# Kernel tuning notes

Hardware: AMD Instinct MI355X
Metric: run time of the kernel (lower is better)

The kernel has to match this reference:

```python
import jax, jax.numpy as jnp
import numpy as np

EPS = 1e-5
K = 20

def _bn(x, g, b, m, v, caxis):
    shape = [1] * x.ndim
    shape[caxis] = x.shape[caxis]
    rs = lambda p: p.reshape(shape)
    return (x - rs(m)) * (rs(g) / jnp.sqrt(rs(v) + EPS)) + rs(b)

def _lrelu(x):
    return jnp.where(x > 0, x, 0.2 * x)

def _graph_feature(x, k):
    # x: [B, C, N] -> [B, N, k, 2C]
    xt = jnp.swapaxes(x, 1, 2)                       # [B, N, C]
    xx = jnp.sum(x * x, axis=1)                      # [B, N]
    dist = xx[:, :, None] + xx[:, None, :] - 2.0 * jnp.einsum('bnc,bmc->bnm', xt, xt)
    _, idx = jax.lax.top_k(-dist, k)                 # smallest distances, [B, N, k]
    nbr = jax.vmap(lambda t, i: t[i])(xt, idx)       # [B, N, k, C]
    center = xt[:, :, None, :]
    return jnp.concatenate([jnp.broadcast_to(center, nbr.shape), nbr - center], axis=-1)

def _edgeconv(x, W, g, b, m, v, k):
    feat = _graph_feature(x, k)                      # [B, N, k, 2C]
    y = jnp.einsum('bnkc,oc->bonk', feat, W)         # 1x1 conv2d
    y = _lrelu(_bn(y, g, b, m, v, caxis=1))
    return jnp.max(y, axis=-1)                       # [B, O, N]


def setup_inputs() -> dict:
    key = jax.random.key(0)
    ks = jax.random.split(key, 40)
    d = {}
    d['x'] = jax.random.normal(ks[0], (8, 3, 2048), dtype=jnp.float32)
    def mk_w(k_, o, i):
        return jax.random.normal(k_, (o, i), dtype=jnp.float32) * (1.0 / np.sqrt(i))
    def mk_bn(k_, c, pfx, out):
        k1, k2, k3, k4 = jax.random.split(k_, 4)
        out[pfx + '_g'] = jax.random.normal(k1, (c,), jnp.float32) * 0.1 + 1.0
        out[pfx + '_b'] = jax.random.normal(k2, (c,), jnp.float32) * 0.1
        out[pfx + '_m'] = jax.random.normal(k3, (c,), jnp.float32) * 0.1
        out[pfx + '_v'] = jax.random.uniform(k4, (c,), jnp.float32) + 0.5
    d['W1'] = mk_w(ks[1], 64, 6);    mk_bn(ks[2], 64, 'bn1', d)
    d['W2'] = mk_w(ks[3], 64, 128);  mk_bn(ks[4], 64, 'bn2', d)
    d['W3'] = mk_w(ks[5], 128, 128); mk_bn(ks[6], 128, 'bn3', d)
    d['W4'] = mk_w(ks[7], 256, 256); mk_bn(ks[8], 256, 'bn4', d)
    d['W5'] = mk_w(ks[9], 1024, 512); mk_bn(ks[10], 1024, 'bn5', d)
    d['L1'] = mk_w(ks[11], 512, 2048); mk_bn(ks[12], 512, 'bn6', d)
    d['L2'] = mk_w(ks[13], 256, 512);  mk_bn(ks[14], 256, 'bn7', d)
    d['L3'] = mk_w(ks[15], 40, 256)
    d['L3_b'] = jax.random.normal(ks[16], (40,), jnp.float32) * 0.01
    return d


def reference(x, W1, bn1_g, bn1_b, bn1_m, bn1_v,
              W2, bn2_g, bn2_b, bn2_m, bn2_v,
              W3, bn3_g, bn3_b, bn3_m, bn3_v,
              W4, bn4_g, bn4_b, bn4_m, bn4_v,
              W5, bn5_g, bn5_b, bn5_m, bn5_v,
              L1, bn6_g, bn6_b, bn6_m, bn6_v,
              L2, bn7_g, bn7_b, bn7_m, bn7_v,
              L3, L3_b):
    x1 = _edgeconv(x,  W1, bn1_g, bn1_b, bn1_m, bn1_v, K)   # [B, 64, N]
    x2 = _edgeconv(x1, W2, bn2_g, bn2_b, bn2_m, bn2_v, K)   # [B, 64, N]
    x3 = _edgeconv(x2, W3, bn3_g, bn3_b, bn3_m, bn3_v, K)   # [B, 128, N]
    x4 = _edgeconv(x3, W4, bn4_g, bn4_b, bn4_m, bn4_v, K)   # [B, 256, N]
    xc = jnp.concatenate([x1, x2, x3, x4], axis=1)          # [B, 512, N]
    emb = _lrelu(_bn(jnp.einsum('bcn,oc->bon', xc, W5), bn5_g, bn5_b, bn5_m, bn5_v, caxis=1))
    feat = jnp.concatenate([jnp.max(emb, axis=-1), jnp.mean(emb, axis=-1)], axis=1)  # [B, 2048]
    h = _lrelu(_bn(feat @ L1.T, bn6_g, bn6_b, bn6_m, bn6_v, caxis=1))
    h = _lrelu(_bn(h @ L2.T, bn7_g, bn7_b, bn7_m, bn7_v, caxis=1))
    return h @ L3.T + L3_b
```

## Files before the change

kernel.cpp:

```cpp
#include <hip/hip_runtime.h>
#include <math.h>

#define NPTS 2048
#define KNN 20
#define EPS_BN 1e-5f

__global__ __launch_bounds__(256) void xx_kernel(const float* __restrict__ xin,
                                                 long bstride,
                                                 float* __restrict__ xx, int C) {
    int b = blockIdx.y;
    int n = blockIdx.x * 256 + threadIdx.x;
    const float* xb = xin + (long)b * bstride;
    float s = 0.f;
    for (int c = 0; c < C; ++c) {
        float v = xb[(long)c * NPTS + n];
        s = fmaf(v, v, s);
    }
    xx[(long)b * NPTS + n] = s;
}

__global__ __launch_bounds__(512) void dist_topk_kernel(const float* __restrict__ xin,
                                                        long bstride,
                                                        const float* __restrict__ xx,
                                                        int* __restrict__ idxout, int C) {
    __shared__ float dist_s[8 * NPTS];
    int b = blockIdx.y;
    int n0 = blockIdx.x * 8;
    int tid = threadIdx.x;
    const float* xb = xin + (long)b * bstride;

    float acc[8][4];
#pragma unroll
    for (int r = 0; r < 8; ++r)
#pragma unroll
        for (int q = 0; q < 4; ++q) acc[r][q] = 0.f;

    for (int c = 0; c < C; ++c) {
        const float* row = xb + (long)c * NPTS;
        float4 xm4 = *(const float4*)(row + 4 * tid);
        float xm[4] = {xm4.x, xm4.y, xm4.z, xm4.w};
#pragma unroll
        for (int r = 0; r < 8; ++r) {
            float xnv = row[n0 + r];
#pragma unroll
            for (int q = 0; q < 4; ++q) acc[r][q] = fmaf(xnv, xm[q], acc[r][q]);
        }
    }

    const float* xxb = xx + (long)b * NPTS;
    float4 xxm4 = *(const float4*)(xxb + 4 * tid);
    float xxm[4] = {xxm4.x, xxm4.y, xxm4.z, xxm4.w};
    float xxn[8];
#pragma unroll
    for (int r = 0; r < 8; ++r) xxn[r] = xxb[n0 + r];

#pragma unroll
    for (int r = 0; r < 8; ++r) {
        float4 d;
        d.x = xxn[r] + xxm[0] - 2.f * acc[r][0];
        d.y = xxn[r] + xxm[1] - 2.f * acc[r][1];
        d.z = xxn[r] + xxm[2] - 2.f * acc[r][2];
        d.w = xxn[r] + xxm[3] - 2.f * acc[r][3];
        *(float4*)(dist_s + r * NPTS + 4 * tid) = d;
    }
    __syncthreads();

    int wave = tid >> 6, lane = tid & 63;
    int n = n0 + wave;
    float v[32];
#pragma unroll
    for (int i = 0; i < 32; ++i) v[i] = dist_s[wave * NPTS + lane + 64 * i];
    int* outp = idxout + ((long)b * NPTS + n) * KNN;

    float* wls = dist_s + wave * NPTS;

    float lm = v[0];
#pragma unroll
    for (int i = 1; i < 32; ++i) lm = fminf(lm, v[i]);
    wls[lane] = lm;
    int rk = 0;
#pragma unroll
    for (int j = 0; j < 64; ++j) {
        float lj = wls[j];
        rk += (lj < lm || (lj == lm && j < lane)) ? 1 : 0;
    }
    unsigned long long bm19 = __ballot(rk == 19);
    int src19 = (int)__ffsll((long long)bm19) - 1;
    float T = __shfl(lm, src19, 64);

    float* cand_v = wls + 256;
    int* cand_i = (int*)(wls + 320);
    int base = 0;
#pragma unroll
    for (int i = 0; i < 32; ++i) {
        bool pred = v[i] <= T;
        unsigned long long mask = __ballot(pred);
        int prefix = __builtin_amdgcn_mbcnt_hi(
            (unsigned)(mask >> 32),
            __builtin_amdgcn_mbcnt_lo((unsigned)mask, 0));
        if (pred) {
            int pos = base + prefix;
            if (pos < 64) { cand_v[pos] = v[i]; cand_i[pos] = lane + 64 * i; }
        }
        base += (int)__popcll(mask);
    }
    int M = base;

    if (M <= 64) {
        bool valid = lane < M;
        float cv = valid ? cand_v[lane] : 0.f;
        int ci = valid ? cand_i[lane] : 0;
        unsigned u = __float_as_uint(cv);
        unsigned su = (u & 0x80000000u) ? ~u : (u | 0x80000000u);
        unsigned long long key =
            valid ? (((unsigned long long)su << 32) | (unsigned)ci) : ~0ull;
        unsigned long long* key_s = (unsigned long long*)(wls + 384);
        key_s[lane] = key;
        int rk2 = 0;
#pragma unroll
        for (int j = 0; j < 64; ++j) rk2 += (key_s[j] < key) ? 1 : 0;
        bool win = valid && (rk2 < KNN);
        unsigned long long wm = __ballot(win);
        int prefix = __builtin_amdgcn_mbcnt_hi(
            (unsigned)(wm >> 32),
            __builtin_amdgcn_mbcnt_lo((unsigned)wm, 0));
        if (win) outp[prefix] = ci;
    } else {
        for (int kk = 0; kk < KNN; ++kk) {
            float bv = v[0];
            int bi = 0;
#pragma unroll
            for (int i = 1; i < 32; ++i)
                if (v[i] < bv) { bv = v[i]; bi = i; }
            int bm = lane + 64 * bi;
#pragma unroll
            for (int off = 32; off >= 1; off >>= 1) {
                float ov = __shfl_xor(bv, off, 64);
                int om = __shfl_xor(bm, off, 64);
                if (ov < bv || (ov == bv && om < bm)) { bv = ov; bm = om; }
            }
            if (lane == 0) outp[kk] = bm;
#pragma unroll
            for (int i = 0; i < 32; ++i)
                if (bm == lane + 64 * i) v[i] = 3.0e38f;
        }
    }
}

__global__ __launch_bounds__(256) void gemm_tu_kernel(
    const float* __restrict__ xin, long bstride, const float* __restrict__ W,
    const float* __restrict__ bg, const float* __restrict__ bb,
    const float* __restrict__ bm, const float* __restrict__ bv,
    float* __restrict__ tbuf, float* __restrict__ ubuf, int C, int O) {
    __shared__ float wa_s[128 * 16];
    __shared__ float wb_s[128 * 16];
    int b = blockIdx.z;
    int o0 = blockIdx.y * 16;
    int n0 = blockIdx.x * 256;
    int tid = threadIdx.x;

    for (int i = tid; i < C * 16; i += 256) {
        int c = i >> 4, ol = i & 15;
        float w1 = W[(long)(o0 + ol) * (2 * C) + c];
        float w2 = W[(long)(o0 + ol) * (2 * C) + C + c];
        wa_s[i] = w1 - w2;
        wb_s[i] = w2;
    }
    __syncthreads();

    float ta[16], ua[16];
#pragma unroll
    for (int ol = 0; ol < 16; ++ol) { ta[ol] = 0.f; ua[ol] = 0.f; }

    const float* xb = xin + (long)b * bstride;
    for (int c = 0; c < C; ++c) {
        float xv = xb[(long)c * NPTS + n0 + tid];
        const float* wac = wa_s + c * 16;
        const float* wbc = wb_s + c * 16;
#pragma unroll
        for (int ol = 0; ol < 16; ++ol) {
            ta[ol] = fmaf(wac[ol], xv, ta[ol]);
            ua[ol] = fmaf(wbc[ol], xv, ua[ol]);
        }
    }

#pragma unroll
    for (int ol = 0; ol < 16; ++ol) {
        int o = o0 + ol;
        float sc = bg[o] / sqrtf(bv[o] + EPS_BN);
        float bias = bb[o] - bm[o] * sc;
        long base = ((long)b * O + o) * NPTS + n0 + tid;
        tbuf[base] = ta[ol] * sc + bias;
        ubuf[base] = ua[ol] * sc;
    }
}

__global__ __launch_bounds__(256) void gather_kernel(const float* __restrict__ tbuf,
                                                     const float* __restrict__ ubuf,
                                                     const int* __restrict__ idx,
                                                     float* __restrict__ out, int O) {
    __shared__ float urow[NPTS];
    int o = blockIdx.x, half = blockIdx.y, b = blockIdx.z;
    int tid = threadIdx.x;
    const float4* up4 = (const float4*)(ubuf + ((long)b * O + o) * NPTS);
    float4* ur4 = (float4*)urow;
    for (int i = tid; i < NPTS / 4; i += 256) ur4[i] = up4[i];
    __syncthreads();

    const float* tp = tbuf + ((long)b * O + o) * NPTS;
    float* op = out + (long)b * (512 * NPTS) + (long)o * NPTS;
    int n = half * 1024 + tid * 4;
    float4 tv4 = *(const float4*)(tp + n);
    float tv[4] = {tv4.x, tv4.y, tv4.z, tv4.w};
    float res[4];
#pragma unroll
    for (int q = 0; q < 4; ++q) {
        const int4* ip = (const int4*)(idx + ((long)b * NPTS + n + q) * KNN);
        float mx = -3.0e38f;
#pragma unroll
        for (int jj = 0; jj < 5; ++jj) {
            int4 i4 = ip[jj];
            float y0 = tv[q] + urow[i4.x];
            float y1 = tv[q] + urow[i4.y];
            float y2 = tv[q] + urow[i4.z];
            float y3 = tv[q] + urow[i4.w];
            y0 = y0 > 0.f ? y0 : 0.2f * y0;
            y1 = y1 > 0.f ? y1 : 0.2f * y1;
            y2 = y2 > 0.f ? y2 : 0.2f * y2;
            y3 = y3 > 0.f ? y3 : 0.2f * y3;
            mx = fmaxf(mx, fmaxf(fmaxf(y0, y1), fmaxf(y2, y3)));
        }
        res[q] = mx;
    }
    *(float4*)(op + n) = make_float4(res[0], res[1], res[2], res[3]);
}

__global__ __launch_bounds__(512) void w5_reduce_kernel(
    const float* __restrict__ xc, const float* __restrict__ W5,
    const float* __restrict__ bg, const float* __restrict__ bb,
    const float* __restrict__ bm, const float* __restrict__ bv,
    float* __restrict__ pmax, float* __restrict__ psum) {
    __shared__ float w_s[512 * 16];
    __shared__ float rmax[8][16];
    __shared__ float rsum[8][16];
    int b = blockIdx.z;
    int half = blockIdx.y;
    int o0 = blockIdx.x * 16;
    int tid = threadIdx.x;

    for (int i = tid; i < 512 * 16; i += 512) {
        int c = i >> 4, ol = i & 15;
        w_s[i] = W5[(long)(o0 + ol) * 512 + c];
    }
    __syncthreads();

    float acc[2][16];
#pragma unroll
    for (int v = 0; v < 2; ++v)
#pragma unroll
        for (int ol = 0; ol < 16; ++ol) acc[v][ol] = 0.f;

    const float* xb = xc + (long)b * 512 * NPTS + half * 1024;
    for (int c = 0; c < 512; ++c) {
        float2 xv = *(const float2*)(xb + (long)c * NPTS + 2 * tid);
        const float* wc = w_s + c * 16;
#pragma unroll
        for (int ol = 0; ol < 16; ++ol) {
            float w = wc[ol];
            acc[0][ol] = fmaf(w, xv.x, acc[0][ol]);
            acc[1][ol] = fmaf(w, xv.y, acc[1][ol]);
        }
    }

    float mx[16], sm[16];
#pragma unroll
    for (int ol = 0; ol < 16; ++ol) {
        int o = o0 + ol;
        float sc = bg[o] / sqrtf(bv[o] + EPS_BN);
        float bi = bb[o] - bm[o] * sc;
        float y0 = acc[0][ol] * sc + bi;
        float y1 = acc[1][ol] * sc + bi;
        y0 = y0 > 0.f ? y0 : 0.2f * y0;
        y1 = y1 > 0.f ? y1 : 0.2f * y1;
        mx[ol] = fmaxf(y0, y1);
        sm[ol] = y0 + y1;
    }

    int wave = tid >> 6, lane = tid & 63;
#pragma unroll
    for (int ol = 0; ol < 16; ++ol) {
        float m = mx[ol], s = sm[ol];
#pragma unroll
        for (int off = 32; off >= 1; off >>= 1) {
            m = fmaxf(m, __shfl_xor(m, off, 64));
            s += __shfl_xor(s, off, 64);
        }
        mx[ol] = m;
        sm[ol] = s;
    }
    if (lane == 0) {
#pragma unroll
        for (int ol = 0; ol < 16; ++ol) { rmax[wave][ol] = mx[ol]; rsum[wave][ol] = sm[ol]; }
    }
    __syncthreads();
    if (tid < 16) {
        float m = rmax[0][tid], s = rsum[0][tid];
#pragma unroll
        for (int w = 1; w < 8; ++w) { m = fmaxf(m, rmax[w][tid]); s += rsum[w][tid]; }
        long base = ((long)half * 8 + b) * 1024 + o0 + tid;
        pmax[base] = m;
        psum[base] = s;
    }
}

__global__ __launch_bounds__(256) void w5_combine_kernel(const float* __restrict__ pmax,
                                                         const float* __restrict__ psum,
                                                         float* __restrict__ feat) {
    int b = blockIdx.x;
    for (int o = threadIdx.x; o < 1024; o += 256) {
        float m = fmaxf(pmax[(long)b * 1024 + o], pmax[(long)(8 + b) * 1024 + o]);
        float s = psum[(long)b * 1024 + o] + psum[(long)(8 + b) * 1024 + o];
        feat[(long)b * 2048 + o] = m;
        feat[(long)b * 2048 + 1024 + o] = s * (1.f / 2048.f);
    }
}

__global__ __launch_bounds__(256) void fc_kernel(const float* __restrict__ in,
                                                 const float* __restrict__ W,
                                                 const float* __restrict__ bg,
                                                 const float* __restrict__ bb,
                                                 const float* __restrict__ bm,
                                                 const float* __restrict__ bv,
                                                 float* __restrict__ out, int I, int O,
                                                 int do_lrelu) {
    int b = blockIdx.y;
    int o = blockIdx.x * 4 + (threadIdx.x >> 6);
    int lane = threadIdx.x & 63;
    if (o < O) {
        const float* ip = in + (long)b * I;
        const float* wp = W + (long)o * I;
        float s = 0.f;
        for (int i = lane; i < I; i += 64) s = fmaf(ip[i], wp[i], s);
#pragma unroll
        for (int off = 32; off >= 1; off >>= 1) s += __shfl_xor(s, off, 64);
        if (lane == 0) {
            float y;
            if (bg) {
                float scv = bg[o] / sqrtf(bv[o] + EPS_BN);
                y = (s - bm[o]) * scv + bb[o];
                if (do_lrelu) y = y > 0.f ? y : 0.2f * y;
            } else {
                y = s + bb[o];
            }
            out[(long)b * O + o] = y;
        }
    }
}

extern "C" void kernel_launch(void* const* d_in, const int* in_sizes, int n_in,
                              void* d_out, int out_size, void* d_ws, size_t ws_size,
                              hipStream_t stream) {
    const float* x = (const float*)d_in[0];
    const float* W1 = (const float*)d_in[1];
    const float* W2 = (const float*)d_in[6];
    const float* W3 = (const float*)d_in[11];
    const float* W4 = (const float*)d_in[16];
    const float* W5 = (const float*)d_in[21];
    const float* L1 = (const float*)d_in[26];
    const float* L2 = (const float*)d_in[31];
    const float* L3 = (const float*)d_in[36];
    const float* L3b = (const float*)d_in[37];

    float* xc = (float*)d_ws;
    float* tb = xc + (long)8 * 512 * NPTS;
    float* ub = tb + (long)8 * 256 * NPTS;
    int* idx = (int*)(ub + (long)8 * 256 * NPTS);
    float* xxb = (float*)(idx + (long)8 * NPTS * KNN);
    float* feat = xxb + (long)8 * NPTS;
    float* h1 = feat + (long)8 * NPTS;
    float* h2 = h1 + (long)8 * 512;
    float* pmax = tb;
    float* psum = tb + (long)2 * 8 * 1024;

    struct Layer {
        const float* xin; long bstride; const float* W;
        const float *g, *b, *m, *v; int C, O, c0;
    };
    Layer layers[4] = {
        {x, (long)3 * NPTS, W1,
         (const float*)d_in[2], (const float*)d_in[3], (const float*)d_in[4], (const float*)d_in[5],
         3, 64, 0},
        {xc, (long)512 * NPTS, W2,
         (const float*)d_in[7], (const float*)d_in[8], (const float*)d_in[9], (const float*)d_in[10],
         64, 64, 64},
        {xc + (long)64 * NPTS, (long)512 * NPTS, W3,
         (const float*)d_in[12], (const float*)d_in[13], (const float*)d_in[14], (const float*)d_in[15],
         64, 128, 128},
        {xc + (long)128 * NPTS, (long)512 * NPTS, W4,
         (const float*)d_in[17], (const float*)d_in[18], (const float*)d_in[19], (const float*)d_in[20],
         128, 256, 256},
    };

    for (int l = 0; l < 4; ++l) {
        const Layer& L = layers[l];
        xx_kernel<<<dim3(NPTS / 256, 8), 256, 0, stream>>>(L.xin, L.bstride, xxb, L.C);
        dist_topk_kernel<<<dim3(NPTS / 8, 8), 512, 0, stream>>>(L.xin, L.bstride, xxb, idx, L.C);
        gemm_tu_kernel<<<dim3(NPTS / 256, L.O / 16, 8), 256, 0, stream>>>(
            L.xin, L.bstride, L.W, L.g, L.b, L.m, L.v, tb, ub, L.C, L.O);
        gather_kernel<<<dim3(L.O, 2, 8), 256, 0, stream>>>(tb, ub, idx, xc + (long)L.c0 * NPTS, L.O);
    }

    w5_reduce_kernel<<<dim3(1024 / 16, 2, 8), 512, 0, stream>>>(
        xc, W5, (const float*)d_in[22], (const float*)d_in[23], (const float*)d_in[24],
        (const float*)d_in[25], pmax, psum);
    w5_combine_kernel<<<dim3(8), 256, 0, stream>>>(pmax, psum, feat);

    fc_kernel<<<dim3(512 / 4, 8), 256, 0, stream>>>(
        feat, L1, (const float*)d_in[27], (const float*)d_in[28], (const float*)d_in[29],
        (const float*)d_in[30], h1, 2048, 512, 1);
    fc_kernel<<<dim3(256 / 4, 8), 256, 0, stream>>>(
        h1, L2, (const float*)d_in[32], (const float*)d_in[33], (const float*)d_in[34],
        (const float*)d_in[35], h2, 512, 256, 1);
    fc_kernel<<<dim3(10, 8), 256, 0, stream>>>(
        h2, L3, nullptr, L3b, nullptr, nullptr, (float*)d_out, 256, 40, 0);
}
```

Before: 1.026 ms.

## Run W5 embedding GEMM on bf16 MFMA with split hi/lo precision

Replaces the scalar FP32 W5 reduction kernel with an MFMA-based GEMM that uses a three-product bf16 hi/lo split to approximate FP32 accuracy. It adds kernels that convert W5 and transpose and convert the concatenated features into bf16 hi/lo layouts, plus precomputation of the BN scale and bias. The goal is to move the largest dense matmul onto matrix cores. The cost is extra conversion and transpose passes, more memory traffic for the split operands, and a wider 32-way partial max/sum combine.

```diff
diff --git a/kernel.cpp b/kernel.cpp
--- a/kernel.cpp
+++ b/kernel.cpp
@@ -4,6 +4,18 @@
 #define NPTS 2048
 #define KNN 20
 #define EPS_BN 1e-5f
+
+typedef unsigned short ushort;
+typedef __attribute__((ext_vector_type(8))) short short8;
+typedef __attribute__((ext_vector_type(4))) float float4v;
+
+__device__ inline ushort bf16_rne(float x) {
+    unsigned u = __float_as_uint(x);
+    return (ushort)((u + 0x7fffu + ((u >> 16) & 1u)) >> 16);
+}
+__device__ inline float bf16_to_f(ushort h) {
+    return __uint_as_float(((unsigned)h) << 16);
+}
 
 __global__ __launch_bounds__(256) void xx_kernel(const float* __restrict__ xin,
                                                  long bstride,
@@ -235,81 +247,145 @@
     *(float4*)(op + n) = make_float4(res[0], res[1], res[2], res[3]);
 }
 
-__global__ __launch_bounds__(512) void w5_reduce_kernel(
-    const float* __restrict__ xc, const float* __restrict__ W5,
-    const float* __restrict__ bg, const float* __restrict__ bb,
-    const float* __restrict__ bm, const float* __restrict__ bv,
-    float* __restrict__ pmax, float* __restrict__ psum) {
-    __shared__ float w_s[512 * 16];
-    __shared__ float rmax[8][16];
-    __shared__ float rsum[8][16];
-    int b = blockIdx.z;
-    int half = blockIdx.y;
-    int o0 = blockIdx.x * 16;
+__global__ __launch_bounds__(256) void transpose_convert_kernel(
+    const float* __restrict__ xc, ushort* __restrict__ xh, ushort* __restrict__ xl) {
+    __shared__ float t[32 * 256];
+    int c0 = blockIdx.x * 32, n0 = blockIdx.y * 256, b = blockIdx.z;
     int tid = threadIdx.x;
-
-    for (int i = tid; i < 512 * 16; i += 512) {
-        int c = i >> 4, ol = i & 15;
-        w_s[i] = W5[(long)(o0 + ol) * 512 + c];
+#pragma unroll
+    for (int i = 0; i < 8; ++i) {
+        int fi = i * 256 + tid;
+        int c = fi >> 6, n4 = (fi & 63) * 4;
+        *(float4*)(t + c * 256 + n4) =
+            *(const float4*)(xc + ((long)b * 512 + c0 + c) * NPTS + n0 + n4);
     }
     __syncthreads();
-
-    float acc[2][16];
-#pragma unroll
-    for (int v = 0; v < 2; ++v)
-#pragma unroll
-        for (int ol = 0; ol < 16; ++ol) acc[v][ol] = 0.f;
-
-    const float* xb = xc + (long)b * 512 * NPTS + half * 1024;
-    for (int c = 0; c < 512; ++c) {
-        float2 xv = *(const float2*)(xb + (long)c * NPTS + 2 * tid);
-        const float* wc = w_s + c * 16;
-#pragma unroll
-        for (int ol = 0; ol < 16; ++ol) {
-            float w = wc[ol];
-            acc[0][ol] = fmaf(w, xv.x, acc[0][ol]);
-            acc[1][ol] = fmaf(w, xv.y, acc[1][ol]);
-        }
-    }
-
-    float mx[16], sm[16];
-#pragma unroll
-    for (int ol = 0; ol < 16; ++ol) {
-        int o = o0 + ol;
-        float sc = bg[o] / sqrtf(bv[o] + EPS_BN);
-        float bi = bb[o] - bm[o] * sc;
-        float y0 = acc[0][ol] * sc + bi;
-        float y1 = acc[1][ol] * sc + bi;
-        y0 = y0 > 0.f ? y0 : 0.2f * y0;
-        y1 = y1 > 0.f ? y1 : 0.2f * y1;
-        mx[ol] = fmaxf(y0, y1);
-        sm[ol] = y0 + y1;
-    }
-
+    long obase = ((long)b * NPTS + n0 + tid) * 512 + c0;
+#pragma unroll
+    for (int g = 0; g < 8; ++g) {
+        ushort h4[4], l4[4];
+#pragma unroll
+        for (int j = 0; j < 4; ++j) {
+            float v = t[(g * 4 + j) * 256 + tid];
+            ushort h = bf16_rne(v);
+            h4[j] = h;
+            l4[j] = bf16_rne(v - bf16_to_f(h));
+        }
+        *(ushort4*)(xh + obase + g * 4) = make_ushort4(h4[0], h4[1], h4[2], h4[3]);
+        *(ushort4*)(xl + obase + g * 4) = make_ushort4(l4[0], l4[1], l4[2], l4[3]);
+    }
+}
+
+__global__ __launch_bounds__(256) void w5_convert_kernel(const float* __restrict__ W5,
+                                                         ushort* __restrict__ wh,
+                                                         ushort* __restrict__ wl) {
+    long i4 = ((long)blockIdx.x * 256 + threadIdx.x) * 4;
+    float4 v = *(const float4*)(W5 + i4);
+    float vv[4] = {v.x, v.y, v.z, v.w};
+    ushort h4[4], l4[4];
+#pragma unroll
+    for (int j = 0; j < 4; ++j) {
+        ushort h = bf16_rne(vv[j]);
+        h4[j] = h;
+        l4[j] = bf16_rne(vv[j] - bf16_to_f(h));
+    }
+    *(ushort4*)(wh + i4) = make_ushort4(h4[0], h4[1], h4[2], h4[3]);
+    *(ushort4*)(wl + i4) = make_ushort4(l4[0], l4[1], l4[2], l4[3]);
+}
+
+__global__ __launch_bounds__(256) void prep_scb_kernel(const float* __restrict__ bg,
+                                                       const float* __restrict__ bb,
+                                                       const float* __restrict__ bm,
+                                                       const float* __restrict__ bv,
+                                                       float2* __restrict__ scb) {
+    int o = blockIdx.x * 256 + threadIdx.x;
+    float sc = bg[o] / sqrtf(bv[o] + EPS_BN);
+    scb[o] = make_float2(sc, bb[o] - bm[o] * sc);
+}
+
+__global__ __launch_bounds__(256) void w5_mfma_kernel(
+    const ushort* __restrict__ Wh, const ushort* __restrict__ Wl,
+    const ushort* __restrict__ Xh, const ushort* __restrict__ Xl,
+    const float2* __restrict__ scb, float* __restrict__ pmax,
+    float* __restrict__ psum) {
+    int b = blockIdx.z, nblk = blockIdx.y, oblk = blockIdx.x;
+    int tid = threadIdx.x;
     int wave = tid >> 6, lane = tid & 63;
-#pragma unroll
-    for (int ol = 0; ol < 16; ++ol) {
-        float m = mx[ol], s = sm[ol];
-#pragma unroll
-        for (int off = 32; off >= 1; off >>= 1) {
-            m = fmaxf(m, __shfl_xor(m, off, 64));
-            s += __shfl_xor(s, off, 64);
-        }
-        mx[ol] = m;
-        sm[ol] = s;
-    }
-    if (lane == 0) {
-#pragma unroll
-        for (int ol = 0; ol < 16; ++ol) { rmax[wave][ol] = mx[ol]; rsum[wave][ol] = sm[ol]; }
-    }
-    __syncthreads();
-    if (tid < 16) {
-        float m = rmax[0][tid], s = rsum[0][tid];
-#pragma unroll
-        for (int w = 1; w < 8; ++w) { m = fmaxf(m, rmax[w][tid]); s += rsum[w][tid]; }
-        long base = ((long)half * 8 + b) * 1024 + o0 + tid;
-        pmax[base] = m;
-        psum[base] = s;
+    int osub = wave & 1, nsub = wave >> 1;
+    int o_base = oblk * 128 + osub * 64;
+    int n_base = nblk * 128 + nsub * 64;
+    int l15 = lane & 15, quad = lane >> 4;
+
+    const ushort* Ah = Wh + (long)(o_base + l15) * 512 + quad * 8;
+    const ushort* Al = Wl + (long)(o_base + l15) * 512 + quad * 8;
+    const ushort* Bh = Xh + ((long)b * NPTS + n_base + l15) * 512 + quad * 8;
+    const ushort* Bl = Xl + ((long)b * NPTS + n_base + l15) * 512 + quad * 8;
+
+    float4v acc[4][4];
+#pragma unroll
+    for (int i = 0; i < 4; ++i)
+#pragma unroll
+        for (int j = 0; j < 4; ++j) acc[i][j] = (float4v)(0.f);
+
+    for (int k = 0; k < 16; ++k) {
+        int c0 = k * 32;
+        short8 bh[4], bl[4];
+#pragma unroll
+        for (int tn = 0; tn < 4; ++tn) {
+            bh[tn] = *(const short8*)(Bh + tn * (16 * 512) + c0);
+            bl[tn] = *(const short8*)(Bl + tn * (16 * 512) + c0);
+        }
+#pragma unroll
+        for (int to = 0; to < 4; ++to) {
+            short8 ah = *(const short8*)(Ah + to * (16 * 512) + c0);
+            short8 al = *(const short8*)(Al + to * (16 * 512) + c0);
+#pragma unroll
+            for (int tn = 0; tn < 4; ++tn) {
+                acc[to][tn] =
+                    __builtin_amdgcn_mfma_f32_16x16x32_bf16(ah, bh[tn], acc[to][tn], 0, 0, 0);
+                acc[to][tn] =
+                    __builtin_amdgcn_mfma_f32_16x16x32_bf16(ah, bl[tn], acc[to][tn], 0, 0, 0);
+                acc[to][tn] =
+                    __builtin_amdgcn_mfma_f32_16x16x32_bf16(al, bh[tn], acc[to][tn], 0, 0, 0);
+            }
+        }
+    }
+
+    int pidx = nblk * 2 + nsub;
+#pragma unroll
+    for (int to = 0; to < 4; ++to) {
+        int ob = o_base + to * 16 + quad * 4;
+        float mx[4], sm[4];
+#pragma unroll
+        for (int r = 0; r < 4; ++r) {
+            float2 sb = scb[ob + r];
+            float m = -3.0e38f, s = 0.f;
+#pragma unroll
+            for (int tn = 0; tn < 4; ++tn) {
+                float y = acc[to][tn][r] * sb.x + sb.y;
+                y = y > 0.f ? y : 0.2f * y;
+                m = fmaxf(m, y);
+                s += y;
+            }
+            mx[r] = m;
+            sm[r] = s;
+        }
+#pragma unroll
+        for (int r = 0; r < 4; ++r) {
+#pragma unroll
+            for (int off = 1; off < 16; off <<= 1) {
+                mx[r] = fmaxf(mx[r], __shfl_xor(mx[r], off, 64));
+                sm[r] += __shfl_xor(sm[r], off, 64);
+            }
+        }
+        if (l15 == 0) {
+            long base = ((long)pidx * 8 + b) * 1024 + ob;
+#pragma unroll
+            for (int r = 0; r < 4; ++r) {
+                pmax[base + r] = mx[r];
+                psum[base + r] = sm[r];
+            }
+        }
     }
 }
 
@@ -318,8 +394,11 @@
                                                          float* __restrict__ feat) {
     int b = blockIdx.x;
     for (int o = threadIdx.x; o < 1024; o += 256) {
-        float m = fmaxf(pmax[(long)b * 1024 + o], pmax[(long)(8 + b) * 1024 + o]);
-        float s = psum[(long)b * 1024 + o] + psum[(long)(8 + b) * 1024 + o];
+        float m = -3.0e38f, s = 0.f;
+        for (int p = 0; p < 32; ++p) {
+            m = fmaxf(m, pmax[((long)p * 8 + b) * 1024 + o]);
+            s += psum[((long)p * 8 + b) * 1024 + o];
+        }
         feat[(long)b * 2048 + o] = m;
         feat[(long)b * 2048 + 1024 + o] = s * (1.f / 2048.f);
     }
@@ -379,8 +458,13 @@
     float* feat = xxb + (long)8 * NPTS;
     float* h1 = feat + (long)8 * NPTS;
     float* h2 = h1 + (long)8 * 512;
-    float* pmax = tb;
-    float* psum = tb + (long)2 * 8 * 1024;
+    float* pmax = h2 + (long)8 * 256;
+    float* psum = pmax + (long)32 * 8 * 1024;
+    float2* scb = (float2*)(psum + (long)32 * 8 * 1024);
+    ushort* W5h = (ushort*)(scb + 1024);
+    ushort* W5l = W5h + (long)1024 * 512;
+    ushort* Xh = (ushort*)tb;
+    ushort* Xl = (ushort*)ub;
 
     struct Layer {
         const float* xin; long bstride; const float* W;
@@ -410,9 +494,12 @@
         gather_kernel<<<dim3(L.O, 2, 8), 256, 0, stream>>>(tb, ub, idx, xc + (long)L.c0 * NPTS, L.O);
     }
 
-    w5_reduce_kernel<<<dim3(1024 / 16, 2, 8), 512, 0, stream>>>(
-        xc, W5, (const float*)d_in[22], (const float*)d_in[23], (const float*)d_in[24],
-        (const float*)d_in[25], pmax, psum);
+    w5_convert_kernel<<<dim3(512), 256, 0, stream>>>(W5, W5h, W5l);
+    prep_scb_kernel<<<dim3(4), 256, 0, stream>>>(
+        (const float*)d_in[22], (const float*)d_in[23], (const float*)d_in[24],
+        (const float*)d_in[25], scb);
+    transpose_convert_kernel<<<dim3(16, 8, 8), 256, 0, stream>>>(xc, Xh, Xl);
+    w5_mfma_kernel<<<dim3(8, 16, 8), 256, 0, stream>>>(W5h, W5l, Xh, Xl, scb, pmax, psum);
     w5_combine_kernel<<<dim3(8), 256, 0, stream>>>(pmax, psum, feat);
 
     fc_kernel<<<dim3(512 / 4, 8), 256, 0, stream>>>(
```

Result: faster. 948.7 us (-7.6%).
